# Kernel tuning notes

Measured on AMD Instinct MI355X. Metric: run time of the kernel, lower is better.

## Reference

```python
import jax, jax.numpy as jnp
import numpy as np

N, E, ET = 100000, 1000000, 200000
F, D, H, L = 64, 32, 66, 2
BN_EPS = 1e-5

def _w(key, shape):
    fan_in = shape[-2] if len(shape) >= 2 else shape[-1]
    return jax.random.normal(key, shape, dtype=jnp.float32) / np.sqrt(fan_in)

def setup_inputs() -> dict:
    key = jax.random.key(0)
    ks = jax.random.split(key, 30)
    inp = {
        'x': jax.random.normal(ks[0], (N, F), dtype=jnp.float32),
        'edge_index': jax.random.randint(ks[1], (2, E), 0, N),
        'edge_attr': jax.random.normal(ks[2], (E, D), dtype=jnp.float32),
        'edge_label_index': jax.random.randint(ks[3], (2, ET), 0, N),
        'target_edge_attr': jax.random.normal(ks[4], (ET, D), dtype=jnp.float32),
        # embeddings
        'node_w': _w(ks[5], (F, H)), 'node_b': jnp.zeros((H,), jnp.float32),
        'edge_w': _w(ks[6], (D, H)), 'edge_b': jnp.zeros((H,), jnp.float32),
        # per-layer GINEConv MLP (Linear-ReLU-Linear), stacked over layers
        'conv_w1': _w(ks[7], (L, H, H)), 'conv_b1': jnp.zeros((L, H), jnp.float32),
        'conv_w2': _w(ks[8], (L, H, H)), 'conv_b2': jnp.zeros((L, H), jnp.float32),
        # per-layer BatchNorm affine params
        'bn_gamma': jnp.ones((L, H), jnp.float32), 'bn_beta': jnp.zeros((L, H), jnp.float32),
        # per-layer edge-update MLP (3H -> H -> H)
        'emlp_w1': _w(ks[9], (L, 3 * H, H)), 'emlp_b1': jnp.zeros((L, H), jnp.float32),
        'emlp_w2': _w(ks[10], (L, H, H)), 'emlp_b2': jnp.zeros((L, H), jnp.float32),
        # final classifier MLP (3H -> 50 -> 25 -> 2); dropout treated as eval (identity)
        'mlp_w1': _w(ks[11], (3 * H, 50)), 'mlp_b1': jnp.zeros((50,), jnp.float32),
        'mlp_w2': _w(ks[12], (50, 25)), 'mlp_b2': jnp.zeros((25,), jnp.float32),
        'mlp_w3': _w(ks[13], (25, 2)), 'mlp_b3': jnp.zeros((2,), jnp.float32),
    }
    return inp

def reference(x, edge_attr, target_edge_attr, node_w, node_b, edge_w, edge_b,
              conv_w1, conv_b1, conv_w2, conv_b2, bn_gamma, bn_beta,
              emlp_w1, emlp_b1, emlp_w2, emlp_b2,
              mlp_w1, mlp_b1, mlp_w2, mlp_b2, mlp_w3, mlp_b3,
              edge_index, edge_label_index):
    n = x.shape[0]
    src, dst = edge_index[0], edge_index[1]
    tsrc, tdst = edge_label_index[0], edge_label_index[1]
    h = x @ node_w + node_b              # [N, H]
    ea = edge_attr @ edge_w + edge_b     # [E, H]
    tea = target_edge_attr @ edge_w + edge_b  # [ET, H]
    n_layers = conv_w1.shape[0]
    for i in range(n_layers):
        # GINEConv: (1+eps)*x + sum_j relu(x_j + e_ij), eps=0, then MLP
        msg = jax.nn.relu(h[src] + ea)                               # [E, H]
        aggr = jax.ops.segment_sum(msg, dst, num_segments=n)         # [N, H]
        z = h + aggr
        z = jax.nn.relu(z @ conv_w1[i] + conv_b1[i]) @ conv_w2[i] + conv_b2[i]
        # BatchNorm (training-mode batch stats, biased variance)
        mean = z.mean(axis=0)
        var = jnp.var(z, axis=0)
        z = (z - mean) * jax.lax.rsqrt(var + BN_EPS) * bn_gamma[i] + bn_beta[i]
        h = (h + jax.nn.relu(z)) / 2
        # edge update on target edges
        cat = jnp.concatenate([h[tsrc], h[tdst], tea], axis=-1)      # [ET, 3H]
        upd = jax.nn.relu(cat @ emlp_w1[i] + emlp_b1[i]) @ emlp_w2[i] + emlp_b2[i]
        tea = tea + upd / 2
    pair = jax.nn.relu(jnp.concatenate([h[tsrc], h[tdst]], axis=-1))  # [ET, 2H]
    feat = jnp.concatenate([pair, tea], axis=-1)                      # [ET, 3H]
    o = jax.nn.relu(feat @ mlp_w1 + mlp_b1)
    o = jax.nn.relu(o @ mlp_w2 + mlp_b2)
    return o @ mlp_w3 + mlp_b3
```

## Files before the change

### kernel.cpp

```cpp
#include <hip/hip_runtime.h>

#define NN 100000
#define NE 1000000
#define NT 200000

typedef __attribute__((ext_vector_type(8))) short short8;
typedef __attribute__((ext_vector_type(4))) float f32x4;

__device__ __forceinline__ unsigned short f2b(float x) {
  union { float f; unsigned int u; } v; v.f = x;
  unsigned int r = v.u + 0x7fffu + ((v.u >> 16) & 1u);
  return (unsigned short)(r >> 16);
}

struct WTab { const float* src[17]; int K[17]; int C[17]; };

__global__ __launch_bounds__(256) void prep_w(WTab tab, unsigned short* wT) {
  int b = blockIdx.x;
  const float* src = tab.src[b];
  int K = tab.K[b], C = tab.C[b];
  unsigned short* dst = wT + (size_t)b * 8320;
  for (int i = threadIdx.x; i < 8320; i += 256) {
    int c = i / 104, k = i - c * 104;
    float v = (c < C && k < K) ? src[k * C + c] : 0.0f;
    dst[i] = f2b(v);
  }
}

template<int K, int KSTEPS, int CT, int C, int AIN, int ROUT>
__global__ __launch_bounds__(256) void mfma_gemm(
    const void* __restrict__ in, const float* __restrict__ add,
    const unsigned short* __restrict__ Bt, const float* __restrict__ bias,
    void* __restrict__ outp, int R)
{
  __shared__ __align__(16) unsigned short As[64 * 104];
  __shared__ __align__(16) unsigned short Bs[80 * 104];
  __shared__ float bs[80];
  const int t = threadIdx.x;
  const int r0 = blockIdx.x * 64;
  for (int i = t; i < 1040; i += 256) ((uint4*)Bs)[i] = ((const uint4*)Bt)[i];
  if (t < 80) bs[t] = (bias && t < C) ? bias[t] : 0.0f;
  constexpr int KH = KSTEPS * 16;
  for (int i = t; i < 64 * KH; i += 256) {
    int r = i / KH, kk = (i - r * KH) * 2;
    int rg = r0 + r;
    unsigned short u0 = 0, u1 = 0;
    if (rg < R && kk < K) {
      if constexpr (AIN == 3) {
        unsigned int u = ((const unsigned int*)in)[((size_t)rg * K + kk) >> 1];
        u0 = u & 0xffffu; u1 = u >> 16;
      } else {
        float2 f = *(const float2*)((const float*)in + (size_t)rg * K + kk);
        float v0 = f.x, v1 = f.y;
        if constexpr (AIN == 1) {
          float2 g = *(const float2*)(add + (size_t)rg * K + kk);
          v0 += g.x; v1 += g.y;
        }
        if constexpr (AIN == 2) { v0 = fmaxf(v0, 0.f); v1 = fmaxf(v1, 0.f); }
        u0 = f2b(v0); u1 = f2b(v1);
      }
    }
    As[r * 104 + kk] = u0; As[r * 104 + kk + 1] = u1;
  }
  __syncthreads();
  const int lane = t & 63, w = t >> 6, m = lane & 15, q = lane >> 4;
  f32x4 acc[CT] = {};
  const unsigned short* Ap = As + (w * 16 + m) * 104 + q * 8;
  const unsigned short* Bp = Bs + m * 104 + q * 8;
#pragma unroll
  for (int ks = 0; ks < KSTEPS; ks++) {
    short8 a = *(const short8*)(Ap + ks * 32);
#pragma unroll
    for (int ct = 0; ct < CT; ct++) {
      short8 b = *(const short8*)(Bp + ct * 16 * 104 + ks * 32);
      acc[ct] = __builtin_amdgcn_mfma_f32_16x16x32_bf16(a, b, acc[ct], 0, 0, 0);
    }
  }
#pragma unroll
  for (int ct = 0; ct < CT; ct++) {
    int c = ct * 16 + m;
    if (c < C) {
      float bv = bs[c];
#pragma unroll
      for (int r2 = 0; r2 < 4; r2++) {
        int row = r0 + w * 16 + q * 4 + r2;
        if (row < R) {
          float v = acc[ct][r2] + bv;
          if constexpr ((ROUT & 1) != 0) v = fmaxf(v, 0.f);
          if constexpr ((ROUT & 2) != 0)
            ((unsigned short*)outp)[(size_t)row * C + c] = f2b(v);
          else
            ((float*)outp)[(size_t)row * C + c] = v;
        }
      }
    }
  }
}

__global__ __launch_bounds__(256) void hist_kernel(const int* __restrict__ ei,
                                                   int* __restrict__ deg)
{
  int e = blockIdx.x * 256 + threadIdx.x;
  if (e < NE) atomicAdd(&deg[ei[NE + e]], 1);
}

__global__ __launch_bounds__(1024) void scan_kernel(const int* __restrict__ deg,
                                                    int* __restrict__ rowptr)
{
  __shared__ int sums[1024];
  const int t = threadIdx.x;
  const int CH = (NN + 1023) / 1024;
  int lo = t * CH, hi = lo + CH;
  if (hi > NN) hi = NN;
  int s = 0;
  for (int i = lo; i < hi; i++) s += deg[i];
  sums[t] = s;
  __syncthreads();
  for (int off = 1; off < 1024; off <<= 1) {
    int v = (t >= off) ? sums[t - off] : 0;
    __syncthreads();
    sums[t] += v;
    __syncthreads();
  }
  int run = (t == 0) ? 0 : sums[t - 1];
  for (int i = lo; i < hi; i++) { rowptr[i] = run; run += deg[i]; }
  if (t == 1023) rowptr[NN] = run;
}

__global__ __launch_bounds__(256) void fill_kernel(
    const int* __restrict__ ei, const int* __restrict__ rowptr,
    int* __restrict__ cur, int* __restrict__ srcS, int* __restrict__ dstS,
    int* __restrict__ permS)
{
  int e = blockIdx.x * 256 + threadIdx.x;
  if (e >= NE) return;
  int d = ei[NE + e];
  int pos = atomicAdd(&cur[d], 1);
  int w = rowptr[d] + pos;
  srcS[w] = ei[e];
  dstS[w] = d;
  permS[w] = e;
}

__global__ __launch_bounds__(256) void perm_eattr(
    const float* __restrict__ eattr, const int* __restrict__ permS,
    unsigned short* __restrict__ eaB)
{
  int i = blockIdx.x * 256 + threadIdx.x;
  if (i >= NE * 32) return;
  int w = i >> 5, k = i & 31;
  eaB[i] = f2b(eattr[(size_t)permS[w] * 32 + k]);
}

__global__ __launch_bounds__(256) void msg_aggr2(
    const int* __restrict__ rowptr, const int* __restrict__ srcS,
    const int* __restrict__ dstS, const unsigned short* __restrict__ eaB,
    const float* __restrict__ eattr, const int* __restrict__ permS,
    const unsigned short* __restrict__ Bt, const float* __restrict__ bias,
    const float* __restrict__ h, float* __restrict__ aggr)
{
  __shared__ __align__(16) unsigned short As[64 * 40];
  __shared__ __align__(16) unsigned short Bs[80 * 104];
  __shared__ float msgS[64 * 67];
  __shared__ float bs[80];
  __shared__ int sidx[64], didx[64];
  const int t = threadIdx.x;
  const int e0 = blockIdx.x * 64;
  for (int i = t; i < 1040; i += 256) ((uint4*)Bs)[i] = ((const uint4*)Bt)[i];
  if (t < 80) bs[t] = (t < 66) ? bias[t] : 0.0f;
  if (t < 64) { sidx[t] = srcS[e0 + t]; didx[t] = dstS[e0 + t]; }
  if (eaB) {
    for (int i = t; i < 1024; i += 256) {
      int r = i >> 4, j = i & 15;
      unsigned int u = ((const unsigned int*)eaB)[(size_t)(e0 + r) * 16 + j];
      As[r * 40 + j * 2] = u & 0xffffu;
      As[r * 40 + j * 2 + 1] = u >> 16;
    }
  } else {
    for (int i = t; i < 1024; i += 256) {
      int r = i >> 4, j = i & 15;
      int p = permS[e0 + r];
      float2 f = ((const float2*)(eattr + (size_t)p * 32))[j];
      As[r * 40 + j * 2] = f2b(f.x);
      As[r * 40 + j * 2 + 1] = f2b(f.y);
    }
  }
  __syncthreads();
  const int lane = t & 63, w = t >> 6, m = lane & 15, q = lane >> 4;
  f32x4 acc[5] = {};
  short8 a = *(const short8*)(As + (w * 16 + m) * 40 + q * 8);
#pragma unroll
  for (int ct = 0; ct < 5; ct++) {
    short8 b = *(const short8*)(Bs + (ct * 16 + m) * 104 + q * 8);
    acc[ct] = __builtin_amdgcn_mfma_f32_16x16x32_bf16(a, b, acc[ct], 0, 0, 0);
  }
#pragma unroll
  for (int ct = 0; ct < 5; ct++) {
    int c = ct * 16 + m;
    if (c < 66) {
      float bv = bs[c];
#pragma unroll
      for (int r2 = 0; r2 < 4; r2++) {
        int e = w * 16 + q * 4 + r2;
        float v = acc[ct][r2] + bv + h[(size_t)sidx[e] * 66 + c];
        msgS[e * 67 + c] = fmaxf(v, 0.f);
      }
    }
  }
  __syncthreads();
  if (t < 66) {
    const int nfirst = didx[0], nlast = didx[63];
    const bool fp = rowptr[nfirst] < e0;
    const bool lp = rowptr[nlast + 1] > e0 + 64;
    float s = 0.0f;
    for (int e = 0; e < 64; e++) {
      s += msgS[e * 67 + t];
      bool bound = (e == 63) || (didx[e + 1] != didx[e]);
      if (bound) {
        int n = didx[e];
        if ((n == nfirst && fp) || (n == nlast && lp))
          atomicAdd(&aggr[(size_t)n * 66 + t], s);
        else
          aggr[(size_t)n * 66 + t] = s;
        s = 0.0f;
      }
    }
  }
}

__global__ __launch_bounds__(256) void bn_stats(const float* __restrict__ z,
                                                float* __restrict__ stat)
{
  const int t = threadIdx.x;
  if (t >= 198) return;
  const int c = t % 66, rs = t / 66;
  const int r0 = blockIdx.x * 1024;
  float s1 = 0.0f, s2 = 0.0f;
  int rend = r0 + 1024; if (rend > NN) rend = NN;
  for (int r = r0 + rs; r < rend; r += 3) {
    float v = z[(size_t)r * 66 + c];
    s1 += v; s2 += v * v;
  }
  atomicAdd(&stat[c], s1);
  atomicAdd(&stat[66 + c], s2);
}

__global__ __launch_bounds__(256) void bn_update(
    float* __restrict__ h, const float* __restrict__ z,
    const float* __restrict__ stat,
    const float* __restrict__ gamma, const float* __restrict__ beta)
{
  int idx = blockIdx.x * 256 + threadIdx.x;
  if (idx >= NN * 66) return;
  int c = idx % 66;
  float mean = stat[c] * (1.0f / NN);
  float var  = stat[66 + c] * (1.0f / NN) - mean * mean;
  float inv  = rsqrtf(var + 1e-5f);
  float zn   = (z[idx] - mean) * inv * gamma[c] + beta[c];
  h[idx] = 0.5f * (h[idx] + fmaxf(zn, 0.0f));
}

__global__ __launch_bounds__(256) void edge_fused2(
    const float* __restrict__ P1, const float* __restrict__ P2,
    const int* __restrict__ eli, const unsigned short* __restrict__ B1t,
    const float* __restrict__ b1, const unsigned short* __restrict__ B2t,
    const float* __restrict__ b2, float* __restrict__ tea)
{
  __shared__ __align__(16) unsigned short As[64 * 104];
  __shared__ __align__(16) unsigned short Bs1[80 * 104];
  __shared__ __align__(16) unsigned short Bs2[80 * 104];
  __shared__ float b1s[80], b2s[80];
  __shared__ int sidx[64], didx[64];
  const int t = threadIdx.x;
  const int e0 = blockIdx.x * 64;
  for (int i = t; i < 1040; i += 256) {
    ((uint4*)Bs1)[i] = ((const uint4*)B1t)[i];
    ((uint4*)Bs2)[i] = ((const uint4*)B2t)[i];
  }
  if (t < 80) { b1s[t] = (t < 66) ? b1[t] : 0.f; b2s[t] = (t < 66) ? b2[t] : 0.f; }
  if (t < 64) { sidx[t] = eli[e0 + t]; didx[t] = eli[NT + e0 + t]; }
  for (int i = t; i < 64 * 48; i += 256) {
    int r = i / 48, kk = (i - r * 48) * 2;
    unsigned short u0 = 0, u1 = 0;
    if (kk < 66) {
      float2 f = *(const float2*)(tea + (size_t)(e0 + r) * 66 + kk);
      u0 = f2b(f.x); u1 = f2b(f.y);
    }
    As[r * 104 + kk] = u0; As[r * 104 + kk + 1] = u1;
  }
  __syncthreads();
  const int lane = t & 63, w = t >> 6, m = lane & 15, q = lane >> 4;
  const unsigned short* Ap = As + (w * 16 + m) * 104 + q * 8;
  const unsigned short* Bp1 = Bs1 + m * 104 + q * 8;
  f32x4 acc[5] = {};
#pragma unroll
  for (int ks = 0; ks < 3; ks++) {
    short8 a = *(const short8*)(Ap + ks * 32);
#pragma unroll
    for (int ct = 0; ct < 5; ct++) {
      short8 b = *(const short8*)(Bp1 + ct * 16 * 104 + ks * 32);
      acc[ct] = __builtin_amdgcn_mfma_f32_16x16x32_bf16(a, b, acc[ct], 0, 0, 0);
    }
  }
  __syncthreads();
#pragma unroll
  for (int ct = 0; ct < 5; ct++) {
    int c = ct * 16 + m;
    if (c < 66) {
      float bv = b1s[c];
#pragma unroll
      for (int r2 = 0; r2 < 4; r2++) {
        int e = w * 16 + q * 4 + r2;
        float v = acc[ct][r2] + bv + P1[(size_t)sidx[e] * 66 + c]
                                   + P2[(size_t)didx[e] * 66 + c];
        As[e * 104 + c] = f2b(fmaxf(v, 0.f));
      }
    }
  }
  __syncthreads();
  const unsigned short* Bp2 = Bs2 + m * 104 + q * 8;
  f32x4 acc2[5] = {};
#pragma unroll
  for (int ks = 0; ks < 3; ks++) {
    short8 a = *(const short8*)(Ap + ks * 32);
#pragma unroll
    for (int ct = 0; ct < 5; ct++) {
      short8 b = *(const short8*)(Bp2 + ct * 16 * 104 + ks * 32);
      acc2[ct] = __builtin_amdgcn_mfma_f32_16x16x32_bf16(a, b, acc2[ct], 0, 0, 0);
    }
  }
#pragma unroll
  for (int ct = 0; ct < 5; ct++) {
    int c = ct * 16 + m;
    if (c < 66) {
      float bv = b2s[c];
#pragma unroll
      for (int r2 = 0; r2 < 4; r2++) {
        int e = w * 16 + q * 4 + r2;
        size_t idx = (size_t)(e0 + e) * 66 + c;
        tea[idx] += 0.5f * (acc2[ct][r2] + bv);
      }
    }
  }
}

__global__ __launch_bounds__(256) void final_fused2(
    const float* __restrict__ tea, const float* __restrict__ P1f,
    const float* __restrict__ P2f, const int* __restrict__ eli,
    const unsigned short* __restrict__ B1t, const float* __restrict__ b1,
    const float* __restrict__ w2, const float* __restrict__ b2,
    const float* __restrict__ w3, const float* __restrict__ b3,
    float* __restrict__ out)
{
  __shared__ __align__(16) unsigned short As[64 * 104];
  __shared__ __align__(16) unsigned short Bs[64 * 104];
  __shared__ float o1s[64 * 51];
  __shared__ float o2s[64 * 25];
  __shared__ float w2s[50 * 25], w3s[50];
  __shared__ float b1s[64], b2s[25], b3s[2];
  __shared__ int sidx[64], didx[64];
  const int t = threadIdx.x;
  const int e0 = blockIdx.x * 64;
  for (int i = t; i < 832; i += 256) ((uint4*)Bs)[i] = ((const uint4*)B1t)[i];
  for (int i = t; i < 50 * 25; i += 256) w2s[i] = w2[i];
  if (t < 50) { w3s[t] = w3[t]; }
  if (t < 64) { b1s[t] = (t < 50) ? b1[t] : 0.f; sidx[t] = eli[e0 + t]; didx[t] = eli[NT + e0 + t]; }
  if (t < 25) b2s[t] = b2[t];
  if (t < 2)  b3s[t] = b3[t];
  for (int i = t; i < 64 * 48; i += 256) {
    int r = i / 48, kk = (i - r * 48) * 2;
    unsigned short u0 = 0, u1 = 0;
    if (kk < 66) {
      float2 f = *(const float2*)(tea + (size_t)(e0 + r) * 66 + kk);
      u0 = f2b(f.x); u1 = f2b(f.y);
    }
    As[r * 104 + kk] = u0; As[r * 104 + kk + 1] = u1;
  }
  __syncthreads();
  const int lane = t & 63, w = t >> 6, m = lane & 15, q = lane >> 4;
  const unsigned short* Ap = As + (w * 16 + m) * 104 + q * 8;
  const unsigned short* Bp = Bs + m * 104 + q * 8;
  f32x4 acc[4] = {};
#pragma unroll
  for (int ks = 0; ks < 3; ks++) {
    short8 a = *(const short8*)(Ap + ks * 32);
#pragma unroll
    for (int ct = 0; ct < 4; ct++) {
      short8 b = *(const short8*)(Bp + ct * 16 * 104 + ks * 32);
      acc[ct] = __builtin_amdgcn_mfma_f32_16x16x32_bf16(a, b, acc[ct], 0, 0, 0);
    }
  }
#pragma unroll
  for (int ct = 0; ct < 4; ct++) {
    int c = ct * 16 + m;
    if (c < 50) {
      float bv = b1s[c];
#pragma unroll
      for (int r2 = 0; r2 < 4; r2++) {
        int e = w * 16 + q * 4 + r2;
        float v = acc[ct][r2] + bv + P1f[(size_t)sidx[e] * 50 + c]
                                   + P2f[(size_t)didx[e] * 50 + c];
        o1s[e * 51 + c] = fmaxf(v, 0.f);
      }
    }
  }
  __syncthreads();
  for (int it = t; it < 64 * 25; it += 256) {
    int e = it / 25, c = it - e * 25;
    float s = b2s[c];
    for (int k = 0; k < 50; k++) s = fmaf(o1s[e * 51 + k], w2s[k * 25 + c], s);
    o2s[e * 25 + c] = fmaxf(s, 0.f);
  }
  __syncthreads();
  if (t < 128) {
    int e = t >> 1, c = t & 1;
    float s = b3s[c];
    for (int k = 0; k < 25; k++) s = fmaf(o2s[e * 25 + k], w3s[k * 2 + c], s);
    out[(size_t)(e0 + e) * 2 + c] = s;
  }
}

extern "C" void kernel_launch(void* const* d_in, const int* in_sizes, int n_in,
                              void* d_out, int out_size, void* d_ws, size_t ws_size,
                              hipStream_t stream) {
  const float* x      = (const float*)d_in[0];
  const int*   ei     = (const int*)  d_in[1];
  const float* eattr  = (const float*)d_in[2];
  const int*   eli    = (const int*)  d_in[3];
  const float* tattr  = (const float*)d_in[4];
  const float* node_w = (const float*)d_in[5];
  const float* node_b = (const float*)d_in[6];
  const float* edge_w = (const float*)d_in[7];
  const float* edge_b = (const float*)d_in[8];
  const float* cw1    = (const float*)d_in[9];
  const float* cb1    = (const float*)d_in[10];
  const float* cw2    = (const float*)d_in[11];
  const float* cb2    = (const float*)d_in[12];
  const float* bng    = (const float*)d_in[13];
  const float* bnb    = (const float*)d_in[14];
  const float* ew1    = (const float*)d_in[15];
  const float* eb1    = (const float*)d_in[16];
  const float* ew2    = (const float*)d_in[17];
  const float* eb2    = (const float*)d_in[18];
  const float* mw1    = (const float*)d_in[19];
  const float* mb1    = (const float*)d_in[20];
  const float* mw2    = (const float*)d_in[21];
  const float* mb2    = (const float*)d_in[22];
  const float* mw3    = (const float*)d_in[23];
  const float* mb3    = (const float*)d_in[24];
  float* out = (float*)d_out;

  char* p = (char*)d_ws;
  auto alloc = [&](size_t bytes) { void* r = p; p += (bytes + 255) & ~(size_t)255; return r; };
  float* h      = (float*)alloc((size_t)NN * 66 * 4);
  float* buf1   = (float*)alloc((size_t)NN * 66 * 4);
  float* buf2   = (float*)alloc((size_t)NN * 66 * 4);
  float* tea    = (float*)alloc((size_t)NT * 66 * 4);
  float* stat   = (float*)alloc(1024);
  int*   rowptr = (int*)alloc((NN + 1) * 4);
  int*   cur    = (int*)alloc((size_t)NN * 4);
  int*   srcS   = (int*)alloc((size_t)NE * 4);
  int*   dstS   = (int*)alloc((size_t)NE * 4);
  int*   permS  = (int*)alloc((size_t)NE * 4);
  unsigned short* wT = (unsigned short*)alloc((size_t)17 * 8320 * 2);
  size_t used = (size_t)(p - (char*)d_ws);
  unsigned short* eaB = nullptr;
  if (ws_size >= used + (size_t)NE * 32 * 2 + 256)
    eaB = (unsigned short*)alloc((size_t)NE * 32 * 2);

  const int gN = (NN + 63) / 64;
  const int gT = NT / 64;
  const int gE = NE / 64;
  auto slot = [&](int i) { return wT + (size_t)i * 8320; };

  hipMemsetAsync(cur, 0, (size_t)NN * sizeof(int), stream);
  hist_kernel<<<(NE + 255) / 256, 256, 0, stream>>>(ei, cur);
  scan_kernel<<<1, 1024, 0, stream>>>(cur, rowptr);
  hipMemsetAsync(cur, 0, (size_t)NN * sizeof(int), stream);
  fill_kernel<<<(NE + 255) / 256, 256, 0, stream>>>(ei, rowptr, cur, srcS, dstS, permS);
  if (eaB)
    perm_eattr<<<(NE * 32) / 256, 256, 0, stream>>>(eattr, permS, eaB);

  WTab tab;
  tab.src[0] = node_w; tab.K[0] = 64; tab.C[0] = 66;
  tab.src[1] = edge_w; tab.K[1] = 32; tab.C[1] = 66;
  for (int l = 0; l < 2; l++) {
    tab.src[2 + l] = cw1 + (size_t)l * 4356; tab.K[2 + l] = 66; tab.C[2 + l] = 66;
    tab.src[4 + l] = cw2 + (size_t)l * 4356; tab.K[4 + l] = 66; tab.C[4 + l] = 66;
    for (int j = 0; j < 3; j++) {
      tab.src[6 + 3 * l + j] = ew1 + (size_t)l * 13068 + (size_t)j * 4356;
      tab.K[6 + 3 * l + j] = 66; tab.C[6 + 3 * l + j] = 66;
    }
    tab.src[12 + l] = ew2 + (size_t)l * 4356; tab.K[12 + l] = 66; tab.C[12 + l] = 66;
  }
  for (int j = 0; j < 3; j++) {
    tab.src[14 + j] = mw1 + (size_t)j * 3300; tab.K[14 + j] = 66; tab.C[14 + j] = 50;
  }
  prep_w<<<17, 256, 0, stream>>>(tab, wT);

  mfma_gemm<64, 2, 5, 66, 0, 0><<<gN, 256, 0, stream>>>(x, nullptr, slot(0), node_b, h, NN);
  mfma_gemm<32, 1, 5, 66, 0, 0><<<gT, 256, 0, stream>>>(tattr, nullptr, slot(1), edge_b, tea, NT);

  for (int l = 0; l < 2; l++) {
    hipMemsetAsync(buf1, 0, (size_t)NN * 66 * sizeof(float), stream);
    msg_aggr2<<<gE, 256, 0, stream>>>(rowptr, srcS, dstS, eaB, eattr, permS,
                                      slot(1), edge_b, h, buf1);
    mfma_gemm<66, 3, 5, 66, 1, 3><<<gN, 256, 0, stream>>>(
        h, buf1, slot(2 + l), cb1 + l * 66, (unsigned short*)buf2, NN);
    mfma_gemm<66, 3, 5, 66, 3, 0><<<gN, 256, 0, stream>>>(
        (unsigned short*)buf2, nullptr, slot(4 + l), cb2 + l * 66, buf1, NN);
    hipMemsetAsync(stat, 0, 132 * sizeof(float), stream);
    bn_stats<<<(NN + 1023) / 1024, 256, 0, stream>>>(buf1, stat);
    bn_update<<<(NN * 66 + 255) / 256, 256, 0, stream>>>(h, buf1, stat,
                                                         bng + l * 66, bnb + l * 66);
    mfma_gemm<66, 3, 5, 66, 0, 0><<<gN, 256, 0, stream>>>(h, nullptr, slot(6 + 3 * l), nullptr, buf1, NN);
    mfma_gemm<66, 3, 5, 66, 0, 0><<<gN, 256, 0, stream>>>(h, nullptr, slot(7 + 3 * l), nullptr, buf2, NN);
    edge_fused2<<<gT, 256, 0, stream>>>(buf1, buf2, eli, slot(8 + 3 * l), eb1 + l * 66,
                                        slot(12 + l), eb2 + l * 66, tea);
  }

  mfma_gemm<66, 3, 4, 50, 2, 0><<<gN, 256, 0, stream>>>(h, nullptr, slot(14), nullptr, buf1, NN);
  mfma_gemm<66, 3, 4, 50, 2, 0><<<gN, 256, 0, stream>>>(h, nullptr, slot(15), nullptr, buf2, NN);
  final_fused2<<<gT, 256, 0, stream>>>(tea, buf1, buf2, eli, slot(16), mb1,
                                       mw2, mb2, mw3, mb3, out);
}
```

Measured before the change: 1.569 ms.

## Parallelize CSR scan, merge paired node GEMMs, gather bf16 h, parallel run reduction

The single-block 1024-thread scan becomes a three-kernel multi-block scan. The paired per-node projection GEMMs (src/dst halves of the edge MLP and final MLP) are merged into one wider GEMM writing interleaved outputs. A bf16 copy of h is kept for the message gather. The edge-attribute permutation now reads coalesced and scatters through an inverse permutation. The segment reduction in msg_aggr2 is spread over runs×channels instead of 66 serial threads. This trades extra launches and bf16 rounding of h in messages for less bandwidth and more parallelism.

```diff
diff --git a/kernel.cpp b/kernel.cpp
--- a/kernel.cpp
+++ b/kernel.cpp
@@ -3,6 +3,7 @@
 #define NN 100000
 #define NE 1000000
 #define NT 200000
+#define SCB 391
 
 typedef __attribute__((ext_vector_type(8))) short short8;
 typedef __attribute__((ext_vector_type(4))) float f32x4;
@@ -12,17 +13,30 @@
   unsigned int r = v.u + 0x7fffu + ((v.u >> 16) & 1u);
   return (unsigned short)(r >> 16);
 }
-
-struct WTab { const float* src[17]; int K[17]; int C[17]; };
-
-__global__ __launch_bounds__(256) void prep_w(WTab tab, unsigned short* wT) {
-  int b = blockIdx.x;
-  const float* src = tab.src[b];
-  int K = tab.K[b], C = tab.C[b];
-  unsigned short* dst = wT + (size_t)b * 8320;
-  for (int i = threadIdx.x; i < 8320; i += 256) {
+__device__ __forceinline__ float b2f(unsigned short x) {
+  union { unsigned int u; float f; } v; v.u = ((unsigned int)x) << 16;
+  return v.f;
+}
+
+struct PrepTab {
+  const float* a[14]; const float* b[14];
+  int K[14], C[14], rows[14], off[14];
+};
+
+__global__ __launch_bounds__(256) void prep_w(PrepTab tab, unsigned short* wT) {
+  int s = blockIdx.x;
+  const float* A = tab.a[s];
+  const float* B = tab.b[s];
+  int K = tab.K[s], C = tab.C[s], rows = tab.rows[s];
+  unsigned short* dst = wT + tab.off[s];
+  int n = rows * 104;
+  for (int i = threadIdx.x; i < n; i += 256) {
     int c = i / 104, k = i - c * 104;
-    float v = (c < C && k < K) ? src[k * C + c] : 0.0f;
+    float v = 0.0f;
+    if (k < K) {
+      if (c < C) v = A[k * C + c];
+      else if (B && c < 2 * C) v = B[k * C + (c - C)];
+    }
     dst[i] = f2b(v);
   }
 }
@@ -31,15 +45,16 @@
 __global__ __launch_bounds__(256) void mfma_gemm(
     const void* __restrict__ in, const float* __restrict__ add,
     const unsigned short* __restrict__ Bt, const float* __restrict__ bias,
-    void* __restrict__ outp, int R)
-{
+    void* __restrict__ outp, void* __restrict__ out2, int R)
+{
+  constexpr int CR = CT * 16;
   __shared__ __align__(16) unsigned short As[64 * 104];
-  __shared__ __align__(16) unsigned short Bs[80 * 104];
-  __shared__ float bs[80];
+  __shared__ __align__(16) unsigned short Bs[CR * 104];
+  __shared__ float bs[CR];
   const int t = threadIdx.x;
   const int r0 = blockIdx.x * 64;
-  for (int i = t; i < 1040; i += 256) ((uint4*)Bs)[i] = ((const uint4*)Bt)[i];
-  if (t < 80) bs[t] = (bias && t < C) ? bias[t] : 0.0f;
+  for (int i = t; i < CT * 208; i += 256) ((uint4*)Bs)[i] = ((const uint4*)Bt)[i];
+  if (t < CR) bs[t] = (bias && t < C) ? bias[t] : 0.0f;
   constexpr int KH = KSTEPS * 16;
   for (int i = t; i < 64 * KH; i += 256) {
     int r = i / KH, kk = (i - r * KH) * 2;
@@ -91,6 +106,8 @@
             ((unsigned short*)outp)[(size_t)row * C + c] = f2b(v);
           else
             ((float*)outp)[(size_t)row * C + c] = v;
+          if constexpr ((ROUT & 4) != 0)
+            ((unsigned short*)out2)[(size_t)row * C + c] = f2b(v);
         }
       }
     }
@@ -104,33 +121,61 @@
   if (e < NE) atomicAdd(&deg[ei[NE + e]], 1);
 }
 
-__global__ __launch_bounds__(1024) void scan_kernel(const int* __restrict__ deg,
-                                                    int* __restrict__ rowptr)
-{
-  __shared__ int sums[1024];
-  const int t = threadIdx.x;
-  const int CH = (NN + 1023) / 1024;
-  int lo = t * CH, hi = lo + CH;
-  if (hi > NN) hi = NN;
-  int s = 0;
-  for (int i = lo; i < hi; i++) s += deg[i];
-  sums[t] = s;
-  __syncthreads();
-  for (int off = 1; off < 1024; off <<= 1) {
-    int v = (t >= off) ? sums[t - off] : 0;
+__global__ __launch_bounds__(256) void blocksum_k(const int* __restrict__ deg,
+                                                  int* __restrict__ bsum)
+{
+  __shared__ int red[256];
+  const int t = threadIdx.x;
+  int i = blockIdx.x * 256 + t;
+  red[t] = (i < NN) ? deg[i] : 0;
+  __syncthreads();
+  for (int s = 128; s > 0; s >>= 1) {
+    if (t < s) red[t] += red[t + s];
     __syncthreads();
-    sums[t] += v;
+  }
+  if (t == 0) bsum[blockIdx.x] = red[0];
+}
+
+__global__ __launch_bounds__(512) void scansums_k(int* __restrict__ bsum,
+                                                  int* __restrict__ rowptr)
+{
+  __shared__ int s[512];
+  const int t = threadIdx.x;
+  s[t] = (t < SCB) ? bsum[t] : 0;
+  __syncthreads();
+  for (int off = 1; off < 512; off <<= 1) {
+    int v = (t >= off) ? s[t - off] : 0;
     __syncthreads();
-  }
-  int run = (t == 0) ? 0 : sums[t - 1];
-  for (int i = lo; i < hi; i++) { rowptr[i] = run; run += deg[i]; }
-  if (t == 1023) rowptr[NN] = run;
+    s[t] += v;
+    __syncthreads();
+  }
+  if (t < SCB) bsum[t] = (t == 0) ? 0 : s[t - 1];
+  if (t == 0) rowptr[NN] = NE;
+}
+
+__global__ __launch_bounds__(256) void scatter_scan_k(
+    const int* __restrict__ deg, const int* __restrict__ bsum,
+    int* __restrict__ rowptr)
+{
+  __shared__ int s[256];
+  const int t = threadIdx.x;
+  int i = blockIdx.x * 256 + t;
+  int v = (i < NN) ? deg[i] : 0;
+  s[t] = v;
+  __syncthreads();
+  for (int off = 1; off < 256; off <<= 1) {
+    int x = (t >= off) ? s[t - off] : 0;
+    __syncthreads();
+    s[t] += x;
+    __syncthreads();
+  }
+  if (i < NN) rowptr[i] = bsum[blockIdx.x] + s[t] - v;
 }
 
 __global__ __launch_bounds__(256) void fill_kernel(
     const int* __restrict__ ei, const int* __restrict__ rowptr,
     int* __restrict__ cur, int* __restrict__ srcS, int* __restrict__ dstS,
-    int* __restrict__ permS)
+    int* __restrict__ permS, int* __restrict__ invp)
 {
   int e = blockIdx.x * 256 + threadIdx.x;
   if (e >= NE) return;
@@ -140,16 +185,19 @@
   srcS[w] = ei[e];
   dstS[w] = d;
   permS[w] = e;
+  invp[e] = w;
 }
 
 __global__ __launch_bounds__(256) void perm_eattr(
-    const float* __restrict__ eattr, const int* __restrict__ permS,
+    const float* __restrict__ eattr, const int* __restrict__ invp,
     unsigned short* __restrict__ eaB)
 {
   int i = blockIdx.x * 256 + threadIdx.x;
-  if (i >= NE * 32) return;
-  int w = i >> 5, k = i & 31;
-  eaB[i] = f2b(eattr[(size_t)permS[w] * 32 + k]);
+  if (i >= NE * 16) return;
+  int e = i >> 4, j = i & 15;
+  float2 f = ((const float2*)eattr)[i];
+  unsigned int packed = (unsigned int)f2b(f.x) | ((unsigned int)f2b(f.y) << 16);
+  ((unsigned int*)eaB)[(size_t)invp[e] * 16 + j] = packed;
 }
 
 __global__ __launch_bounds__(256) void msg_aggr2(
@@ -157,13 +205,15 @@
     const int* __restrict__ dstS, const unsigned short* __restrict__ eaB,
     const float* __restrict__ eattr, const int* __restrict__ permS,
     const unsigned short* __restrict__ Bt, const float* __restrict__ bias,
-    const float* __restrict__ h, float* __restrict__ aggr)
+    const unsigned short* __restrict__ hB, float* __restrict__ aggr)
 {
   __shared__ __align__(16) unsigned short As[64 * 40];
   __shared__ __align__(16) unsigned short Bs[80 * 104];
   __shared__ float msgS[64 * 67];
   __shared__ float bs[80];
   __shared__ int sidx[64], didx[64];
+  __shared__ int runStart[65];
+  __shared__ int nrunsS;
   const int t = threadIdx.x;
   const int e0 = blockIdx.x * 64;
   for (int i = t; i < 1040; i += 256) ((uint4*)Bs)[i] = ((const uint4*)Bt)[i];
@@ -186,6 +236,13 @@
     }
   }
   __syncthreads();
+  if (t < 64) {
+    bool b = (t == 0) || (didx[t] != didx[t - 1]);
+    unsigned long long mask = __ballot(b);
+    int idx = __popcll(mask & ((1ull << t) - 1ull));
+    if (b) runStart[idx] = t;
+    if (t == 63) { nrunsS = __popcll(mask); runStart[__popcll(mask)] = 64; }
+  }
   const int lane = t & 63, w = t >> 6, m = lane & 15, q = lane >> 4;
   f32x4 acc[5] = {};
   short8 a = *(const short8*)(As + (w * 16 + m) * 40 + q * 8);
@@ -202,29 +259,24 @@
 #pragma unroll
       for (int r2 = 0; r2 < 4; r2++) {
         int e = w * 16 + q * 4 + r2;
-        float v = acc[ct][r2] + bv + h[(size_t)sidx[e] * 66 + c];
+        float v = acc[ct][r2] + bv + b2f(hB[(size_t)sidx[e] * 66 + c]);
         msgS[e * 67 + c] = fmaxf(v, 0.f);
       }
     }
   }
   __syncthreads();
-  if (t < 66) {
-    const int nfirst = didx[0], nlast = didx[63];
-    const bool fp = rowptr[nfirst] < e0;
-    const bool lp = rowptr[nlast + 1] > e0 + 64;
+  const int nr = nrunsS;
+  for (int task = t; task < nr * 66; task += 256) {
+    int r = task / 66, c = task - r * 66;
+    int s0 = runStart[r], s1 = runStart[r + 1];
     float s = 0.0f;
-    for (int e = 0; e < 64; e++) {
-      s += msgS[e * 67 + t];
-      bool bound = (e == 63) || (didx[e + 1] != didx[e]);
-      if (bound) {
-        int n = didx[e];
-        if ((n == nfirst && fp) || (n == nlast && lp))
-          atomicAdd(&aggr[(size_t)n * 66 + t], s);
-        else
-          aggr[(size_t)n * 66 + t] = s;
-        s = 0.0f;
-      }
-    }
+    for (int e = s0; e < s1; e++) s += msgS[e * 67 + c];
+    int n = didx[s0];
+    bool partial = false;
+    if (r == 0)      partial = (rowptr[n] < e0);
+    if (r == nr - 1) partial = partial || (rowptr[n + 1] > e0 + 64);
+    if (partial) atomicAdd(&aggr[(size_t)n * 66 + c], s);
+    else         aggr[(size_t)n * 66 + c] = s;
   }
 }
 
@@ -246,8 +298,8 @@
 }
 
 __global__ __launch_bounds__(256) void bn_update(
-    float* __restrict__ h, const float* __restrict__ z,
-    const float* __restrict__ stat,
+    float* __restrict__ h, unsigned short* __restrict__ hB,
+    const float* __restrict__ z, const float* __restrict__ stat,
     const float* __restrict__ gamma, const float* __restrict__ beta)
 {
   int idx = blockIdx.x * 256 + threadIdx.x;
@@ -257,14 +309,16 @@
   float var  = stat[66 + c] * (1.0f / NN) - mean * mean;
   float inv  = rsqrtf(var + 1e-5f);
   float zn   = (z[idx] - mean) * inv * gamma[c] + beta[c];
-  h[idx] = 0.5f * (h[idx] + fmaxf(zn, 0.0f));
+  float v = 0.5f * (h[idx] + fmaxf(zn, 0.0f));
+  h[idx] = v;
+  hB[idx] = f2b(v);
 }
 
 __global__ __launch_bounds__(256) void edge_fused2(
-    const float* __restrict__ P1, const float* __restrict__ P2,
-    const int* __restrict__ eli, const unsigned short* __restrict__ B1t,
-    const float* __restrict__ b1, const unsigned short* __restrict__ B2t,
-    const float* __restrict__ b2, float* __restrict__ tea)
+    const float* __restrict__ P12, const int* __restrict__ eli,
+    const unsigned short* __restrict__ B1t, const float* __restrict__ b1,
+    const unsigned short* __restrict__ B2t, const float* __restrict__ b2,
+    float* __restrict__ tea)
 {
   __shared__ __align__(16) unsigned short As[64 * 104];
   __shared__ __align__(16) unsigned short Bs1[80 * 104];
@@ -311,8 +365,8 @@
 #pragma unroll
       for (int r2 = 0; r2 < 4; r2++) {
         int e = w * 16 + q * 4 + r2;
-        float v = acc[ct][r2] + bv + P1[(size_t)sidx[e] * 66 + c]
-                                   + P2[(size_t)didx[e] * 66 + c];
+        float v = acc[ct][r2] + bv + P12[(size_t)sidx[e] * 132 + c]
+                                   + P12[(size_t)didx[e] * 132 + 66 + c];
         As[e * 104 + c] = f2b(fmaxf(v, 0.f));
       }
     }
@@ -345,12 +399,11 @@
 }
 
 __global__ __launch_bounds__(256) void final_fused2(
-    const float* __restrict__ tea, const float* __restrict__ P1f,
-    const float* __restrict__ P2f, const int* __restrict__ eli,
-    const unsigned short* __restrict__ B1t, const float* __restrict__ b1,
-    const float* __restrict__ w2, const float* __restrict__ b2,
-    const float* __restrict__ w3, const float* __restrict__ b3,
-    float* __restrict__ out)
+    const float* __restrict__ tea, const float* __restrict__ P12f,
+    const int* __restrict__ eli, const unsigned short* __restrict__ B1t,
+    const float* __restrict__ b1, const float* __restrict__ w2,
+    const float* __restrict__ b2, const float* __restrict__ w3,
+    const float* __restrict__ b3, float* __restrict__ out)
 {
   __shared__ __align__(16) unsigned short As[64 * 104];
   __shared__ __align__(16) unsigned short Bs[64 * 104];
@@ -363,7 +416,7 @@
   const int e0 = blockIdx.x * 64;
   for (int i = t; i < 832; i += 256) ((uint4*)Bs)[i] = ((const uint4*)B1t)[i];
   for (int i = t; i < 50 * 25; i += 256) w2s[i] = w2[i];
-  if (t < 50) { w3s[t] = w3[t]; }
+  if (t < 50) w3s[t] = w3[t];
   if (t < 64) { b1s[t] = (t < 50) ? b1[t] : 0.f; sidx[t] = eli[e0 + t]; didx[t] = eli[NT + e0 + t]; }
   if (t < 25) b2s[t] = b2[t];
   if (t < 2)  b3s[t] = b3[t];
@@ -398,8 +451,8 @@
 #pragma unroll
       for (int r2 = 0; r2 < 4; r2++) {
         int e = w * 16 + q * 4 + r2;
-        float v = acc[ct][r2] + bv + P1f[(size_t)sidx[e] * 50 + c]
-                                   + P2f[(size_t)didx[e] * 50 + c];
+        float v = acc[ct][r2] + bv + P12f[(size_t)sidx[e] * 100 + c]
+                                   + P12f[(size_t)didx[e] * 100 + 50 + c];
         o1s[e * 51 + c] = fmaxf(v, 0.f);
       }
     }
@@ -453,16 +506,19 @@
   char* p = (char*)d_ws;
   auto alloc = [&](size_t bytes) { void* r = p; p += (bytes + 255) & ~(size_t)255; return r; };
   float* h      = (float*)alloc((size_t)NN * 66 * 4);
-  float* buf1   = (float*)alloc((size_t)NN * 66 * 4);
-  float* buf2   = (float*)alloc((size_t)NN * 66 * 4);
+  unsigned short* hB = (unsigned short*)alloc((size_t)NN * 66 * 2);
+  float* big    = (float*)alloc((size_t)NN * 132 * 4);
+  float* zbuf   = (float*)alloc((size_t)NN * 66 * 4);
   float* tea    = (float*)alloc((size_t)NT * 66 * 4);
   float* stat   = (float*)alloc(1024);
   int*   rowptr = (int*)alloc((NN + 1) * 4);
   int*   cur    = (int*)alloc((size_t)NN * 4);
+  int*   bsum   = (int*)alloc((SCB + 1) * 4);
   int*   srcS   = (int*)alloc((size_t)NE * 4);
   int*   dstS   = (int*)alloc((size_t)NE * 4);
   int*   permS  = (int*)alloc((size_t)NE * 4);
-  unsigned short* wT = (unsigned short*)alloc((size_t)17 * 8320 * 2);
+  int*   invp   = (int*)alloc((size_t)NE * 4);
+  unsigned short* wT = (unsigned short*)alloc((size_t)140000 * 2);
   size_t used = (size_t)(p - (char*)d_ws);
   unsigned short* eaB = nullptr;
   if (ws_size >= used + (size_t)NE * 32 * 2 + 256)
@@ -471,56 +527,63 @@
   const int gN = (NN + 63) / 64;
   const int gT = NT / 64;
   const int gE = NE / 64;
-  auto slot = [&](int i) { return wT + (size_t)i * 8320; };
 
   hipMemsetAsync(cur, 0, (size_t)NN * sizeof(int), stream);
   hist_kernel<<<(NE + 255) / 256, 256, 0, stream>>>(ei, cur);
-  scan_kernel<<<1, 1024, 0, stream>>>(cur, rowptr);
+  blocksum_k<<<SCB, 256, 0, stream>>>(cur, bsum);
+  scansums_k<<<1, 512, 0, stream>>>(bsum, rowptr);
+  scatter_scan_k<<<SCB, 256, 0, stream>>>(cur, bsum, rowptr);
   hipMemsetAsync(cur, 0, (size_t)NN * sizeof(int), stream);
-  fill_kernel<<<(NE + 255) / 256, 256, 0, stream>>>(ei, rowptr, cur, srcS, dstS, permS);
+  fill_kernel<<<(NE + 255) / 256, 256, 0, stream>>>(ei, rowptr, cur, srcS, dstS, permS, invp);
   if (eaB)
-    perm_eattr<<<(NE * 32) / 256, 256, 0, stream>>>(eattr, permS, eaB);
-
-  WTab tab;
-  tab.src[0] = node_w; tab.K[0] = 64; tab.C[0] = 66;
-  tab.src[1] = edge_w; tab.K[1] = 32; tab.C[1] = 66;
+    perm_eattr<<<(NE * 16 + 255) / 256, 256, 0, stream>>>(eattr, invp, eaB);
+
+  PrepTab tb;
+  int offs[14];
+  int off = 0;
+  auto set = [&](int s, const float* A, const float* B, int K, int C, int rows) {
+    tb.a[s] = A; tb.b[s] = B; tb.K[s] = K; tb.C[s] = C; tb.rows[s] = rows;
+    tb.off[s] = off; offs[s] = off; off += rows * 104;
+  };
+  set(0, node_w, nullptr, 64, 66, 80);
+  set(1, edge_w, nullptr, 32, 66, 80);
   for (int l = 0; l < 2; l++) {
-    tab.src[2 + l] = cw1 + (size_t)l * 4356; tab.K[2 + l] = 66; tab.C[2 + l] = 66;
-    tab.src[4 + l] = cw2 + (size_t)l * 4356; tab.K[4 + l] = 66; tab.C[4 + l] = 66;
-    for (int j = 0; j < 3; j++) {
-      tab.src[6 + 3 * l + j] = ew1 + (size_t)l * 13068 + (size_t)j * 4356;
-      tab.K[6 + 3 * l + j] = 66; tab.C[6 + 3 * l + j] = 66;
-    }
-    tab.src[12 + l] = ew2 + (size_t)l * 4356; tab.K[12 + l] = 66; tab.C[12 + l] = 66;
-  }
-  for (int j = 0; j < 3; j++) {
-    tab.src[14 + j] = mw1 + (size_t)j * 3300; tab.K[14 + j] = 66; tab.C[14 + j] = 50;
-  }
-  prep_w<<<17, 256, 0, stream>>>(tab, wT);
-
-  mfma_gemm<64, 2, 5, 66, 0, 0><<<gN, 256, 0, stream>>>(x, nullptr, slot(0), node_b, h, NN);
-  mfma_gemm<32, 1, 5, 66, 0, 0><<<gT, 256, 0, stream>>>(tattr, nullptr, slot(1), edge_b, tea, NT);
+    set(2 + l, cw1 + (size_t)l * 4356, nullptr, 66, 66, 80);
+    set(4 + l, cw2 + (size_t)l * 4356, nullptr, 66, 66, 80);
+    set(6 + l, ew1 + (size_t)l * 13068 + 8712, nullptr, 66, 66, 80);
+    set(8 + l, ew2 + (size_t)l * 4356, nullptr, 66, 66, 80);
+    set(10 + l, ew1 + (size_t)l * 13068, ew1 + (size_t)l * 13068 + 4356,
+        66, 66, 144);
+  }
+  set(12, mw1, mw1 + 3300, 66, 50, 112);
+  set(13, mw1 + 6600, nullptr, 66, 50, 80);
+  prep_w<<<14, 256, 0, stream>>>(tb, wT);
+
+  mfma_gemm<64, 2, 5, 66, 0, 4><<<gN, 256, 0, stream>>>(
+      x, nullptr, wT + offs[0], node_b, h, hB, NN);
+  mfma_gemm<32, 1, 5, 66, 0, 0><<<gT, 256, 0, stream>>>(
+      tattr, nullptr, wT + offs[1], edge_b, tea, nullptr, NT);
 
   for (int l = 0; l < 2; l++) {
-    hipMemsetAsync(buf1, 0, (size_t)NN * 66 * sizeof(float), stream);
+    hipMemsetAsync(zbuf, 0, (size_t)NN * 66 * sizeof(float), stream);
     msg_aggr2<<<gE, 256, 0, stream>>>(rowptr, srcS, dstS, eaB, eattr, permS,
-                                      slot(1), edge_b, h, buf1);
+                                      wT + offs[1], edge_b, hB, zbuf);
     mfma_gemm<66, 3, 5, 66, 1, 3><<<gN, 256, 0, stream>>>(
-        h, buf1, slot(2 + l), cb1 + l * 66, (unsigned short*)buf2, NN);
+        h, zbuf, wT + offs[2 + l], cb1 + l * 66, (unsigned short*)big, nullptr, NN);
     mfma_gemm<66, 3, 5, 66, 3, 0><<<gN, 256, 0, stream>>>(
-        (unsigned short*)buf2, nullptr, slot(4 + l), cb2 + l * 66, buf1, NN);
+        (unsigned short*)big, nullptr, wT + offs[4 + l], cb2 + l * 66, zbuf, nullptr, NN);
     hipMemsetAsync(stat, 0, 132 * sizeof(float), stream);
-    bn_stats<<<(NN + 1023) / 1024, 256, 0, stream>>>(buf1, stat);
-    bn_update<<<(NN * 66 + 255) / 256, 256, 0, stream>>>(h, buf1, stat,
+    bn_stats<<<(NN + 1023) / 1024, 256, 0, stream>>>(zbuf, stat);
+    bn_update<<<(NN * 66 + 255) / 256, 256, 0, stream>>>(h, hB, zbuf, stat,
                                                          bng + l * 66, bnb + l * 66);
-    mfma_gemm<66, 3, 5, 66, 0, 0><<<gN, 256, 0, stream>>>(h, nullptr, slot(6 + 3 * l), nullptr, buf1, NN);
-    mfma_gemm<66, 3, 5, 66, 0, 0><<<gN, 256, 0, stream>>>(h, nullptr, slot(7 + 3 * l), nullptr, buf2, NN);
-    edge_fused2<<<gT, 256, 0, stream>>>(buf1, buf2, eli, slot(8 + 3 * l), eb1 + l * 66,
-                                        slot(12 + l), eb2 + l * 66, tea);
-  }
-
-  mfma_gemm<66, 3, 4, 50, 2, 0><<<gN, 256, 0, stream>>>(h, nullptr, slot(14), nullptr, buf1, NN);
-  mfma_gemm<66, 3, 4, 50, 2, 0><<<gN, 256, 0, stream>>>(h, nullptr, slot(15), nullptr, buf2, NN);
-  final_fused2<<<gT, 256, 0, stream>>>(tea, buf1, buf2, eli, slot(16), mb1,
+    mfma_gemm<66, 3, 9, 132, 0, 0><<<gN, 256, 0, stream>>>(
+        h, nullptr, wT + offs[10 + l], nullptr, big, nullptr, NN);
+    edge_fused2<<<gT, 256, 0, stream>>>(big, eli, wT + offs[6 + l], eb1 + l * 66,
+                                        wT + offs[8 + l], eb2 + l * 66, tea);
+  }
+
+  mfma_gemm<66, 3, 7, 100, 2, 0><<<gN, 256, 0, stream>>>(
+      h, nullptr, wT + offs[12], nullptr, big, nullptr, NN);
+  final_fused2<<<gT, 256, 0, stream>>>(tea, big, eli, wT + offs[13], mb1,
                                        mw2, mb2, mw3, mb3, out);
 }
```

Measured after the change: 1.284 ms. 18.1% less time.
